# Kernel optimization log

Hardware: AMD Instinct MI355X
Metric: run time of the kernel (lower is better)

Reference implementation:

```python
import jax, jax.numpy as jnp
import numpy as np

NFEAT, NHID, NCLASS = 256, 128, 40
N_NODES, N_EDGES = 50000, 800000
BN_EPS = 1e-5


def setup_inputs() -> dict:
    key = jax.random.key(0)
    ks = jax.random.split(key, 8)
    x = jax.random.normal(ks[0], (N_NODES, NFEAT), dtype=jnp.float32)
    edge_index = jax.random.randint(ks[1], (2, N_EDGES), 0, N_NODES, dtype=jnp.int64)
    # GCNConv layer 0: nfeat -> nhid (Glorot-ish scale)
    W0 = jax.random.normal(ks[2], (NFEAT, NHID), dtype=jnp.float32) / np.sqrt(NFEAT)
    b0 = jnp.zeros((NHID,), dtype=jnp.float32)
    # BatchNorm1d(nhid)
    gamma0 = jnp.ones((NHID,), dtype=jnp.float32)
    beta0 = jnp.zeros((NHID,), dtype=jnp.float32)
    # GCNConv last: nhid -> nclass
    W1 = jax.random.normal(ks[3], (NHID, NCLASS), dtype=jnp.float32) / np.sqrt(NHID)
    b1 = jnp.zeros((NCLASS,), dtype=jnp.float32)
    return {"x": x, "edge_index": edge_index, "W0": W0, "b0": b0,
            "gamma0": gamma0, "beta0": beta0, "W1": W1, "b1": b1}


def _gcn_conv(x, src, dst, W, b, num_nodes):
    # normalize=False GCNConv: linear transform then raw sum aggregation src->dst
    h = x @ W                                   # [N, out]
    out = jax.ops.segment_sum(h[src], dst, num_segments=num_nodes)
    return out + b


def reference(x, edge_index, W0, b0, gamma0, beta0, W1, b1):
    N = x.shape[0]
    src, dst = edge_index[0], edge_index[1]
    # layer 0 conv
    h = _gcn_conv(x, src, dst, W0, b0, N)       # [N, nhid]
    # BatchNorm1d (training-mode batch stats, biased variance)
    mu = h.mean(axis=0)
    var = jnp.mean((h - mu) ** 2, axis=0)
    h = gamma0 * (h - mu) * jax.lax.rsqrt(var + BN_EPS) + beta0
    h = jax.nn.relu(h)
    # (dropout skipped: deterministic eval baseline)
    # last conv (early-return path in original forward)
    out = _gcn_conv(h, src, dst, W1, b1, N)     # [N, nclass]
    return out
```

## Files before the change

kernel.cpp:

```cpp
#include <hip/hip_runtime.h>
#include <hip/hip_fp8.h>

#define NFEAT 256
#define NHID 128
#define NCLASS 40
#define NNODES 50000
#define NEDGES 800000
#define BN_EPS 1e-5f
#define NBK 196
#define NBLK 100
#define EPB 8000
#define NW1 6250
#define GEMM1_BLOCKS 1563

typedef __attribute__((ext_vector_type(4))) float f32x4;
typedef __attribute__((ext_vector_type(8))) short bf16x8;

__device__ inline ushort f2bf(float f) {
    uint u = __float_as_uint(f);
    u += 0x7FFF + ((u >> 16) & 1);
    return (ushort)(u >> 16);
}
__device__ inline float bflo(uint v) { return __uint_as_float(v << 16); }
__device__ inline float bfhi(uint v) { return __uint_as_float(v & 0xFFFF0000u); }

__device__ inline uint pk_fp8x4(float a0, float a1, float a2, float a3) {
#if __has_builtin(__builtin_amdgcn_cvt_pk_fp8_f32)
    int u = 0;
    u = __builtin_amdgcn_cvt_pk_fp8_f32(a0, a1, u, false);
    u = __builtin_amdgcn_cvt_pk_fp8_f32(a2, a3, u, true);
    return (uint)u;
#else
    __hip_fp8_e4m3 q0(a0), q1(a1), q2(a2), q3(a3);
    return (uint)q0.__x | ((uint)q1.__x << 8) | ((uint)q2.__x << 16) | ((uint)q3.__x << 24);
#endif
}
__device__ inline float fp8lo(uint v) {
#if __has_builtin(__builtin_amdgcn_cvt_f32_fp8)
    return __builtin_amdgcn_cvt_f32_fp8((int)v, 0);
#else
    __hip_fp8_e4m3 q; q.__x = (__hip_fp8_storage_t)(v & 0xFF); return (float)q;
#endif
}
__device__ inline float fp8hi(uint v) {
#if __has_builtin(__builtin_amdgcn_cvt_f32_fp8)
    return __builtin_amdgcn_cvt_f32_fp8((int)v, 1);
#else
    __hip_fp8_e4m3 q; q.__x = (__hip_fp8_storage_t)((v >> 8) & 0xFF); return (float)q;
#endif
}

__global__ void k_prep(const float* __restrict__ W0, ushort* __restrict__ W0F,
                       const int* __restrict__ ei, int* __restrict__ bcnt,
                       float* __restrict__ stats, int* __restrict__ rowptr) {
    __shared__ int cnt[NBK];
    if (blockIdx.x < 16) {
        if (blockIdx.x == 0) {
            stats[threadIdx.x] = 0.f;
            if (threadIdx.x == 0) rowptr[NNODES] = NEDGES;
        }
        const int t = blockIdx.x * 256 + threadIdx.x;
        const int lane = t & 63;
        const int grp = t >> 6;
        const int kc = grp & 7, fi = grp >> 3;
        const int n = fi * 16 + (lane & 15);
        const int k0 = kc * 32 + (lane >> 4) * 8;
        ushort v[8];
        #pragma unroll
        for (int j = 0; j < 8; ++j) v[j] = f2bf(W0[(k0 + j) * NHID + n]);
        uint4 u;
        u.x = (uint)v[0] | ((uint)v[1] << 16);
        u.y = (uint)v[2] | ((uint)v[3] << 16);
        u.z = (uint)v[4] | ((uint)v[5] << 16);
        u.w = (uint)v[6] | ((uint)v[7] << 16);
        *(uint4*)&W0F[(grp * 64 + lane) * 8] = u;
    } else {
        const int blk = blockIdx.x - 16;
        const int t = threadIdx.x;
        if (t < NBK) cnt[t] = 0;
        __syncthreads();
        const int base = blk * EPB;
        for (int i = t; i < EPB; i += 256)
            atomicAdd(&cnt[ei[NEDGES + base + i] >> 8], 1);
        __syncthreads();
        if (t < NBK) bcnt[blk * NBK + t] = cnt[t];
    }
}

__launch_bounds__(256, 1)
__global__ void k_scatter_gemm1(const int* __restrict__ ei, const int* __restrict__ bcnt,
                                uint* __restrict__ packed,
                                const float* __restrict__ x, const ushort* __restrict__ W0F,
                                uchar* __restrict__ h1) {
    __shared__ int s_sc[256], s_cur[256];
    if (blockIdx.x < NBLK) {
        const int tid = threadIdx.x, blk = blockIdx.x;
        int tot = 0, pre = 0;
        if (tid < NBK) {
            for (int bb = 0; bb < NBLK; ++bb) {
                const int v = bcnt[bb * NBK + tid];
                tot += v;
                if (bb < blk) pre += v;
            }
        }
        s_sc[tid] = tot;
        __syncthreads();
        for (int o = 1; o < 256; o <<= 1) {
            const int v = (tid >= o) ? s_sc[tid - o] : 0;
            __syncthreads();
            s_sc[tid] += v;
            __syncthreads();
        }
        s_cur[tid] = (s_sc[tid] - tot) + pre;
        __syncthreads();
        const int base = blk * EPB;
        for (int i = tid; i < EPB; i += 256) {
            const int src = ei[base + i];
            const int dst = ei[NEDGES + base + i];
            const int pos = atomicAdd(&s_cur[dst >> 8], 1);
            packed[pos] = (uint)src | ((uint)(dst & 255) << 16);
        }
    } else {
        const int gt = (blockIdx.x - NBLK) * 256 + threadIdx.x;
        const int w = gt >> 6;
        if (w >= NW1) return;
        const int lane = gt & 63;
        const int half = w & 1;
        const int node = (w >> 1) * 16 + (lane & 15);
        const int nclamp = node < NNODES ? node : NNODES - 1;
        const float* xg = &x[(long)nclamp * NFEAT + (lane >> 4) * 8];

        float4 xa[8], xb[8];
        #pragma unroll
        for (int kc = 0; kc < 8; ++kc) {
            xa[kc] = *(const float4*)(xg + kc * 32);
            xb[kc] = *(const float4*)(xg + kc * 32 + 4);
        }
        __builtin_amdgcn_sched_barrier(0);
        bf16x8 xf[8];
        #pragma unroll
        for (int kc = 0; kc < 8; ++kc) {
            xf[kc][0]=(short)f2bf(xa[kc].x); xf[kc][1]=(short)f2bf(xa[kc].y);
            xf[kc][2]=(short)f2bf(xa[kc].z); xf[kc][3]=(short)f2bf(xa[kc].w);
            xf[kc][4]=(short)f2bf(xb[kc].x); xf[kc][5]=(short)f2bf(xb[kc].y);
            xf[kc][6]=(short)f2bf(xb[kc].z); xf[kc][7]=(short)f2bf(xb[kc].w);
        }
        __builtin_amdgcn_sched_barrier(0);
        f32x4 acc[4];
        #pragma unroll
        for (int f = 0; f < 4; ++f) acc[f] = (f32x4){0.f, 0.f, 0.f, 0.f};
        const ushort* wbase = &W0F[(size_t)lane * 8];
        #pragma unroll
        for (int kc = 0; kc < 8; ++kc) {
            #pragma unroll
            for (int f = 0; f < 4; ++f) {
                const int grp = (half * 4 + f) * 8 + kc;
                const bf16x8 wf = *(const bf16x8*)&wbase[(size_t)grp * 64 * 8];
                acc[f] = __builtin_amdgcn_mfma_f32_16x16x32_bf16(wf, xf[kc], acc[f], 0, 0, 0);
            }
        }
        if (node < NNODES) {
            const int nq = (lane >> 4) * 4;
            uchar* hp = &h1[(long)node * NHID + half * 64 + nq];
            #pragma unroll
            for (int f = 0; f < 4; ++f)
                *(uint*)&hp[f * 16] = pk_fp8x4(acc[f][0], acc[f][1], acc[f][2], acc[f][3]);
        }
    }
}

__launch_bounds__(256)
__global__ void k_bksort(const uint* __restrict__ packed, const int* __restrict__ bcnt,
                         int* __restrict__ esrc, int* __restrict__ rowptr) {
    __shared__ int s_cnt[256], s_sc[256], s_cur[256];
    __shared__ int s_seg[2];
    const int b = blockIdx.x, tid = threadIdx.x;
    int tot = 0;
    if (tid < NBK)
        for (int bb = 0; bb < NBLK; ++bb) tot += bcnt[bb * NBK + tid];
    s_sc[tid] = tot;
    __syncthreads();
    for (int o = 1; o < 256; o <<= 1) {
        const int v = (tid >= o) ? s_sc[tid - o] : 0;
        __syncthreads();
        s_sc[tid] += v;
        __syncthreads();
    }
    if (tid == b) { s_seg[0] = s_sc[b] - tot; s_seg[1] = s_sc[b]; }
    __syncthreads();
    const int nb = s_seg[0], ne = s_seg[1], n = ne - nb;
    s_cnt[tid] = 0;
    __syncthreads();
    for (int i = tid; i < n; i += 256)
        atomicAdd(&s_cnt[packed[nb + i] >> 16], 1);
    __syncthreads();
    const int v = s_cnt[tid];
    s_sc[tid] = v;
    __syncthreads();
    for (int o = 1; o < 256; o <<= 1) {
        const int tmp = (tid >= o) ? s_sc[tid - o] : 0;
        __syncthreads();
        s_sc[tid] += tmp;
        __syncthreads();
    }
    const int excl = s_sc[tid] - v;
    s_cur[tid] = excl;
    const int node = (b << 8) + tid;
    if (node < NNODES) rowptr[node] = nb + excl;
    __syncthreads();
    for (int i = tid; i < n; i += 256) {
        const uint p = packed[nb + i];
        const int pos = atomicAdd(&s_cur[p >> 16], 1);
        esrc[nb + pos] = (int)(p & 0xFFFFu);
    }
}

__launch_bounds__(256)
__global__ void k_gather1(const int* __restrict__ rowptr, const int* __restrict__ esrc,
                          const uchar* __restrict__ h1, const float* __restrict__ b0,
                          ushort* __restrict__ agg1bf) {
    const int w = (blockIdx.x * blockDim.x + threadIdx.x) >> 6;
    const int lane = threadIdx.x & 63;
    if (w >= NNODES) return;
    const int beg = rowptr[w], end = rowptr[w + 1];
    const int f = lane * 2;
    float2 acc = *(const float2*)&b0[f];
    int i = beg;
    for (; i + 7 < end; i += 8) {
        uint v[8];
        #pragma unroll
        for (int j = 0; j < 8; ++j)
            v[j] = (uint)*(const ushort*)&h1[(long)esrc[i + j] * NHID + f];
        #pragma unroll
        for (int j = 0; j < 8; ++j) { acc.x += fp8lo(v[j]); acc.y += fp8hi(v[j]); }
    }
    for (; i < end; ++i) {
        const uint v = (uint)*(const ushort*)&h1[(long)esrc[i] * NHID + f];
        acc.x += fp8lo(v); acc.y += fp8hi(v);
    }
    const uint u = (uint)f2bf(acc.x) | ((uint)f2bf(acc.y) << 16);
    *(uint*)&agg1bf[(long)w * NHID + f] = u;
}

__global__ void k_bnstats(const ushort* __restrict__ agg1bf,
                          float* __restrict__ sums, float* __restrict__ sumsq) {
    __shared__ float sd[256 * 8], sd2[256 * 8];
    const int t = threadIdx.x;
    const int c8 = (t & 15) * 8;
    const int rr = t >> 4;
    float s[8] = {}, q[8] = {};
    for (int r = blockIdx.x * 16 + rr; r < NNODES; r += gridDim.x * 16) {
        const uint4 u = *(const uint4*)&agg1bf[(long)r * NHID + c8];
        const uint uu[4] = {u.x, u.y, u.z, u.w};
        #pragma unroll
        for (int j = 0; j < 4; ++j) {
            const float a0 = bflo(uu[j]), a1 = bfhi(uu[j]);
            s[2 * j] += a0; s[2 * j + 1] += a1;
            q[2 * j] += a0 * a0; q[2 * j + 1] += a1 * a1;
        }
    }
    #pragma unroll
    for (int j = 0; j < 8; ++j) { sd[t * 8 + j] = s[j]; sd2[t * 8 + j] = q[j]; }
    __syncthreads();
    if (t < 128) {
        const int g = t >> 3, j = t & 7;
        float ss = 0.f, qq = 0.f;
        #pragma unroll
        for (int r = 0; r < 16; ++r) {
            ss += sd[(r * 16 + g) * 8 + j];
            qq += sd2[(r * 16 + g) * 8 + j];
        }
        atomicAdd(&sums[g * 8 + j], ss);
        atomicAdd(&sumsq[g * 8 + j], qq);
    }
}

__launch_bounds__(256)
__global__ void k_gemm2(const ushort* __restrict__ agg1bf, const float* __restrict__ W1,
                        const float* __restrict__ sums, const float* __restrict__ sumsq,
                        const float* __restrict__ gamma, const float* __restrict__ beta,
                        ushort* __restrict__ h2) {
    __shared__ float xs[64 * 132];
    __shared__ float wt[40 * 132];
    __shared__ float s_scale[128], s_shift[128];
    const int t = threadIdx.x;
    const int base = blockIdx.x * 64;

    if (t < NHID) {
        const float mu = sums[t] * (1.f / NNODES);
        float var = sumsq[t] * (1.f / NNODES) - mu * mu;
        var = fmaxf(var, 0.f);
        const float sc = gamma[t] * rsqrtf(var + BN_EPS);
        s_scale[t] = sc;
        s_shift[t] = beta[t] - mu * sc;
    }
    for (int idx = t; idx < NHID * NCLASS; idx += 256) {
        const int c = idx / NCLASS, j = idx % NCLASS;
        wt[j * 132 + c] = W1[idx];
    }
    __syncthreads();
    {
        const int cc = (t & 15) * 8;
        const int rb = t >> 4;
        #pragma unroll
        for (int p = 0; p < 4; ++p) {
            const int row = p * 16 + rb;
            const int g = base + row;
            uint4 u = make_uint4(0u, 0u, 0u, 0u);
            if (g < NNODES) u = *(const uint4*)&agg1bf[(long)g * NHID + cc];
            const uint uu[4] = {u.x, u.y, u.z, u.w};
            #pragma unroll
            for (int q = 0; q < 4; ++q) {
                const int c0 = cc + q * 2;
                const float a0 = bflo(uu[q]), a1 = bfhi(uu[q]);
                xs[row * 132 + c0]     = fmaxf(a0 * s_scale[c0]     + s_shift[c0],     0.f);
                xs[row * 132 + c0 + 1] = fmaxf(a1 * s_scale[c0 + 1] + s_shift[c0 + 1], 0.f);
            }
        }
    }
    __syncthreads();

    const int node = t >> 2;
    const int j0 = (t & 3) * 10;
    float acc[10] = {};
    for (int c4 = 0; c4 < 32; ++c4) {
        const int c = c4 * 4;
        const float4 a = *(const float4*)&xs[node * 132 + c];
        #pragma unroll
        for (int jj = 0; jj < 10; ++jj) {
            const float4 wv = *(const float4*)&wt[(j0 + jj) * 132 + c];
            acc[jj] += a.x * wv.x + a.y * wv.y + a.z * wv.z + a.w * wv.w;
        }
    }
    const int g = base + node;
    if (g < NNODES) {
        #pragma unroll
        for (int p = 0; p < 5; ++p) {
            uint u = (uint)f2bf(acc[2 * p]) | ((uint)f2bf(acc[2 * p + 1]) << 16);
            *(uint*)&h2[(long)g * NCLASS + j0 + 2 * p] = u;
        }
    }
}

__launch_bounds__(256)
__global__ void k_gather2(const int* __restrict__ rowptr, const int* __restrict__ esrc,
                          const ushort* __restrict__ h2, const float* __restrict__ b1,
                          float* __restrict__ out) {
    const int t = threadIdx.x;
    if (t >= 240) return;
    const int node = blockIdx.x * 12 + t / 20;
    if (node >= NNODES) return;
    const int f = (t % 20) * 2;
    const int beg = rowptr[node], end = rowptr[node + 1];
    float2 acc = make_float2(b1[f], b1[f + 1]);
    int i = beg;
    for (; i + 3 < end; i += 4) {
        const uint v0 = *(const uint*)&h2[(long)esrc[i]     * NCLASS + f];
        const uint v1 = *(const uint*)&h2[(long)esrc[i + 1] * NCLASS + f];
        const uint v2 = *(const uint*)&h2[(long)esrc[i + 2] * NCLASS + f];
        const uint v3 = *(const uint*)&h2[(long)esrc[i + 3] * NCLASS + f];
        acc.x += (bflo(v0) + bflo(v1)) + (bflo(v2) + bflo(v3));
        acc.y += (bfhi(v0) + bfhi(v1)) + (bfhi(v2) + bfhi(v3));
    }
    for (; i < end; ++i) {
        const uint v = *(const uint*)&h2[(long)esrc[i] * NCLASS + f];
        acc.x += bflo(v); acc.y += bfhi(v);
    }
    *(float2*)&out[(long)node * NCLASS + f] = acc;
}

extern "C" void kernel_launch(void* const* d_in, const int* in_sizes, int n_in,
                              void* d_out, int out_size, void* d_ws, size_t ws_size,
                              hipStream_t stream) {
    const float* x      = (const float*)d_in[0];
    const int*   ei     = (const int*)d_in[1];
    const float* W0     = (const float*)d_in[2];
    const float* b0     = (const float*)d_in[3];
    const float* gamma0 = (const float*)d_in[4];
    const float* beta0  = (const float*)d_in[5];
    const float* W1     = (const float*)d_in[6];
    const float* b1     = (const float*)d_in[7];
    float* out = (float*)d_out;

    char* ws = (char*)d_ws;
    float* sums  = (float*)ws;
    float* sumsq = sums + 128;
    int* wsI     = (int*)(ws + 4096);
    int* rowptr  = wsI;
    int* esrc    = wsI + 50048;
    int* bcnt    = wsI + 850048;
    ushort* W0F  = (ushort*)(ws + 3563520);
    uchar* h1    = (uchar*)(ws + 3629056);
    ushort* agg1bf = (ushort*)(ws + 16429056);
    uint* packed = (uint*)agg1bf;
    ushort* h2   = (ushort*)h1;

    k_prep<<<16 + NBLK, 256, 0, stream>>>(W0, W0F, ei, bcnt, sums, rowptr);
    k_scatter_gemm1<<<NBLK + GEMM1_BLOCKS, 256, 0, stream>>>(ei, bcnt, packed, x, W0F, h1);
    k_bksort<<<NBK, 256, 0, stream>>>(packed, bcnt, esrc, rowptr);
    k_gather1<<<(NNODES * 64 + 255) / 256, 256, 0, stream>>>(rowptr, esrc, h1, b0, agg1bf);
    k_bnstats<<<256, 256, 0, stream>>>(agg1bf, sums, sumsq);
    k_gemm2<<<(NNODES + 63) / 64, 256, 0, stream>>>(agg1bf, W1, sums, sumsq, gamma0, beta0, h2);
    k_gather2<<<(NNODES + 11) / 12, 256, 0, stream>>>(rowptr, esrc, h2, b1, out);
}
```

Before: 148.4 us.

## Co-schedule GEMM1 with bucket sort and make GEMM1 persistent with register-resident weights

The edge scatter now runs as its own small kernel, and GEMM1 is fused with the per-bucket sort instead of the scatter. The GEMM1 blocks become persistent waves (512 blocks) that load their half of W0 into registers once and loop over node tiles, which removes repeated weight reloads. The intent is to hide the latency-bound sort behind GEMM1 work and cut weight traffic. The cost is heavy register use (32 bf16x8 fragments per lane), which could lower occupancy, and the scatter now runs alone with only 100 blocks.

```diff
diff --git a/kernel.cpp b/kernel.cpp
--- a/kernel.cpp
+++ b/kernel.cpp
@@ -11,7 +11,8 @@
 #define NBLK 100
 #define EPB 8000
 #define NW1 6250
-#define GEMM1_BLOCKS 1563
+#define G1R_BLOCKS 512
+#define G1R_WAVES (G1R_BLOCKS * 4)
 
 typedef __attribute__((ext_vector_type(4))) float f32x4;
 typedef __attribute__((ext_vector_type(8))) short bf16x8;
@@ -87,22 +88,49 @@
     }
 }
 
-__launch_bounds__(256, 1)
-__global__ void k_scatter_gemm1(const int* __restrict__ ei, const int* __restrict__ bcnt,
-                                uint* __restrict__ packed,
-                                const float* __restrict__ x, const ushort* __restrict__ W0F,
-                                uchar* __restrict__ h1) {
+__global__ void k_scatter(const int* __restrict__ ei, const int* __restrict__ bcnt,
+                          uint* __restrict__ packed) {
     __shared__ int s_sc[256], s_cur[256];
-    if (blockIdx.x < NBLK) {
-        const int tid = threadIdx.x, blk = blockIdx.x;
-        int tot = 0, pre = 0;
-        if (tid < NBK) {
-            for (int bb = 0; bb < NBLK; ++bb) {
-                const int v = bcnt[bb * NBK + tid];
-                tot += v;
-                if (bb < blk) pre += v;
-            }
-        }
+    const int tid = threadIdx.x, blk = blockIdx.x;
+    int tot = 0, pre = 0;
+    if (tid < NBK) {
+        for (int bb = 0; bb < NBLK; ++bb) {
+            const int v = bcnt[bb * NBK + tid];
+            tot += v;
+            if (bb < blk) pre += v;
+        }
+    }
+    s_sc[tid] = tot;
+    __syncthreads();
+    for (int o = 1; o < 256; o <<= 1) {
+        const int v = (tid >= o) ? s_sc[tid - o] : 0;
+        __syncthreads();
+        s_sc[tid] += v;
+        __syncthreads();
+    }
+    s_cur[tid] = (s_sc[tid] - tot) + pre;
+    __syncthreads();
+    const int base = blk * EPB;
+    for (int i = tid; i < EPB; i += 256) {
+        const int src = ei[base + i];
+        const int dst = ei[NEDGES + base + i];
+        const int pos = atomicAdd(&s_cur[dst >> 8], 1);
+        packed[pos] = (uint)src | ((uint)(dst & 255) << 16);
+    }
+}
+
+__launch_bounds__(256)
+__global__ void k_sort_gemm1(const uint* __restrict__ packed, const int* __restrict__ bcnt,
+                             int* __restrict__ esrc, int* __restrict__ rowptr,
+                             const float* __restrict__ x, const ushort* __restrict__ W0F,
+                             uchar* __restrict__ h1) {
+    __shared__ int s_cnt[256], s_sc[256], s_cur[256];
+    __shared__ int s_seg[2];
+    if (blockIdx.x < NBK) {
+        const int b = blockIdx.x, tid = threadIdx.x;
+        int tot = 0;
+        if (tid < NBK)
+            for (int bb = 0; bb < NBLK; ++bb) tot += bcnt[bb * NBK + tid];
         s_sc[tid] = tot;
         __syncthreads();
         for (int o = 1; o < 256; o <<= 1) {
@@ -111,107 +139,85 @@
             s_sc[tid] += v;
             __syncthreads();
         }
-        s_cur[tid] = (s_sc[tid] - tot) + pre;
-        __syncthreads();
-        const int base = blk * EPB;
-        for (int i = tid; i < EPB; i += 256) {
-            const int src = ei[base + i];
-            const int dst = ei[NEDGES + base + i];
-            const int pos = atomicAdd(&s_cur[dst >> 8], 1);
-            packed[pos] = (uint)src | ((uint)(dst & 255) << 16);
+        if (tid == b) { s_seg[0] = s_sc[b] - tot; s_seg[1] = s_sc[b]; }
+        __syncthreads();
+        const int nb = s_seg[0], ne = s_seg[1], n = ne - nb;
+        s_cnt[tid] = 0;
+        __syncthreads();
+        for (int i = tid; i < n; i += 256)
+            atomicAdd(&s_cnt[packed[nb + i] >> 16], 1);
+        __syncthreads();
+        const int v = s_cnt[tid];
+        s_sc[tid] = v;
+        __syncthreads();
+        for (int o = 1; o < 256; o <<= 1) {
+            const int tmp = (tid >= o) ? s_sc[tid - o] : 0;
+            __syncthreads();
+            s_sc[tid] += tmp;
+            __syncthreads();
+        }
+        const int excl = s_sc[tid] - v;
+        s_cur[tid] = excl;
+        const int node = (b << 8) + tid;
+        if (node < NNODES) rowptr[node] = nb + excl;
+        __syncthreads();
+        for (int i = tid; i < n; i += 256) {
+            const uint p = packed[nb + i];
+            const int pos = atomicAdd(&s_cur[p >> 16], 1);
+            esrc[nb + pos] = (int)(p & 0xFFFFu);
         }
     } else {
-        const int gt = (blockIdx.x - NBLK) * 256 + threadIdx.x;
-        const int w = gt >> 6;
-        if (w >= NW1) return;
-        const int lane = gt & 63;
-        const int half = w & 1;
-        const int node = (w >> 1) * 16 + (lane & 15);
-        const int nclamp = node < NNODES ? node : NNODES - 1;
-        const float* xg = &x[(long)nclamp * NFEAT + (lane >> 4) * 8];
-
-        float4 xa[8], xb[8];
-        #pragma unroll
-        for (int kc = 0; kc < 8; ++kc) {
-            xa[kc] = *(const float4*)(xg + kc * 32);
-            xb[kc] = *(const float4*)(xg + kc * 32 + 4);
-        }
-        __builtin_amdgcn_sched_barrier(0);
-        bf16x8 xf[8];
-        #pragma unroll
-        for (int kc = 0; kc < 8; ++kc) {
-            xf[kc][0]=(short)f2bf(xa[kc].x); xf[kc][1]=(short)f2bf(xa[kc].y);
-            xf[kc][2]=(short)f2bf(xa[kc].z); xf[kc][3]=(short)f2bf(xa[kc].w);
-            xf[kc][4]=(short)f2bf(xb[kc].x); xf[kc][5]=(short)f2bf(xb[kc].y);
-            xf[kc][6]=(short)f2bf(xb[kc].z); xf[kc][7]=(short)f2bf(xb[kc].w);
-        }
-        __builtin_amdgcn_sched_barrier(0);
-        f32x4 acc[4];
-        #pragma unroll
-        for (int f = 0; f < 4; ++f) acc[f] = (f32x4){0.f, 0.f, 0.f, 0.f};
+        const int wv = threadIdx.x >> 6;
+        const int lane = threadIdx.x & 63;
+        const int W = (blockIdx.x - NBK) * 4 + wv;
+        const int half = W & 1;
         const ushort* wbase = &W0F[(size_t)lane * 8];
-        #pragma unroll
-        for (int kc = 0; kc < 8; ++kc) {
-            #pragma unroll
-            for (int f = 0; f < 4; ++f) {
-                const int grp = (half * 4 + f) * 8 + kc;
-                const bf16x8 wf = *(const bf16x8*)&wbase[(size_t)grp * 64 * 8];
-                acc[f] = __builtin_amdgcn_mfma_f32_16x16x32_bf16(wf, xf[kc], acc[f], 0, 0, 0);
+
+        bf16x8 wf[32];
+        #pragma unroll
+        for (int fi = 0; fi < 4; ++fi)
+            #pragma unroll
+            for (int kc = 0; kc < 8; ++kc)
+                wf[fi * 8 + kc] =
+                    *(const bf16x8*)&wbase[(size_t)(((half * 4 + fi) * 8 + kc) * 64) * 8];
+
+        for (int task = W; task < NW1; task += G1R_WAVES) {
+            const int g = task >> 1;
+            const int node = g * 16 + (lane & 15);
+            const int nclamp = node < NNODES ? node : NNODES - 1;
+            const float* xg = &x[(long)nclamp * NFEAT + (lane >> 4) * 8];
+
+            float4 xa[8], xb[8];
+            #pragma unroll
+            for (int kc = 0; kc < 8; ++kc) {
+                xa[kc] = *(const float4*)(xg + kc * 32);
+                xb[kc] = *(const float4*)(xg + kc * 32 + 4);
             }
-        }
-        if (node < NNODES) {
-            const int nq = (lane >> 4) * 4;
-            uchar* hp = &h1[(long)node * NHID + half * 64 + nq];
-            #pragma unroll
-            for (int f = 0; f < 4; ++f)
-                *(uint*)&hp[f * 16] = pk_fp8x4(acc[f][0], acc[f][1], acc[f][2], acc[f][3]);
-        }
-    }
-}
-
-__launch_bounds__(256)
-__global__ void k_bksort(const uint* __restrict__ packed, const int* __restrict__ bcnt,
-                         int* __restrict__ esrc, int* __restrict__ rowptr) {
-    __shared__ int s_cnt[256], s_sc[256], s_cur[256];
-    __shared__ int s_seg[2];
-    const int b = blockIdx.x, tid = threadIdx.x;
-    int tot = 0;
-    if (tid < NBK)
-        for (int bb = 0; bb < NBLK; ++bb) tot += bcnt[bb * NBK + tid];
-    s_sc[tid] = tot;
-    __syncthreads();
-    for (int o = 1; o < 256; o <<= 1) {
-        const int v = (tid >= o) ? s_sc[tid - o] : 0;
-        __syncthreads();
-        s_sc[tid] += v;
-        __syncthreads();
-    }
-    if (tid == b) { s_seg[0] = s_sc[b] - tot; s_seg[1] = s_sc[b]; }
-    __syncthreads();
-    const int nb = s_seg[0], ne = s_seg[1], n = ne - nb;
-    s_cnt[tid] = 0;
-    __syncthreads();
-    for (int i = tid; i < n; i += 256)
-        atomicAdd(&s_cnt[packed[nb + i] >> 16], 1);
-    __syncthreads();
-    const int v = s_cnt[tid];
-    s_sc[tid] = v;
-    __syncthreads();
-    for (int o = 1; o < 256; o <<= 1) {
-        const int tmp = (tid >= o) ? s_sc[tid - o] : 0;
-        __syncthreads();
-        s_sc[tid] += tmp;
-        __syncthreads();
-    }
-    const int excl = s_sc[tid] - v;
-    s_cur[tid] = excl;
-    const int node = (b << 8) + tid;
-    if (node < NNODES) rowptr[node] = nb + excl;
-    __syncthreads();
-    for (int i = tid; i < n; i += 256) {
-        const uint p = packed[nb + i];
-        const int pos = atomicAdd(&s_cur[p >> 16], 1);
-        esrc[nb + pos] = (int)(p & 0xFFFFu);
+            bf16x8 xf[8];
+            #pragma unroll
+            for (int kc = 0; kc < 8; ++kc) {
+                xf[kc][0]=(short)f2bf(xa[kc].x); xf[kc][1]=(short)f2bf(xa[kc].y);
+                xf[kc][2]=(short)f2bf(xa[kc].z); xf[kc][3]=(short)f2bf(xa[kc].w);
+                xf[kc][4]=(short)f2bf(xb[kc].x); xf[kc][5]=(short)f2bf(xb[kc].y);
+                xf[kc][6]=(short)f2bf(xb[kc].z); xf[kc][7]=(short)f2bf(xb[kc].w);
+            }
+            f32x4 acc[4];
+            #pragma unroll
+            for (int f = 0; f < 4; ++f) acc[f] = (f32x4){0.f, 0.f, 0.f, 0.f};
+            #pragma unroll
+            for (int kc = 0; kc < 8; ++kc)
+                #pragma unroll
+                for (int f = 0; f < 4; ++f)
+                    acc[f] = __builtin_amdgcn_mfma_f32_16x16x32_bf16(wf[f * 8 + kc], xf[kc],
+                                                                     acc[f], 0, 0, 0);
+            if (node < NNODES) {
+                const int nq = (lane >> 4) * 4;
+                uchar* hp = &h1[(long)node * NHID + half * 64 + nq];
+                #pragma unroll
+                for (int f = 0; f < 4; ++f)
+                    *(uint*)&hp[f * 16] = pk_fp8x4(acc[f][0], acc[f][1], acc[f][2], acc[f][3]);
+            }
+        }
     }
 }
 
@@ -396,8 +402,8 @@
     ushort* h2   = (ushort*)h1;
 
     k_prep<<<16 + NBLK, 256, 0, stream>>>(W0, W0F, ei, bcnt, sums, rowptr);
-    k_scatter_gemm1<<<NBLK + GEMM1_BLOCKS, 256, 0, stream>>>(ei, bcnt, packed, x, W0F, h1);
-    k_bksort<<<NBK, 256, 0, stream>>>(packed, bcnt, esrc, rowptr);
+    k_scatter<<<NBLK, 256, 0, stream>>>(ei, bcnt, packed);
+    k_sort_gemm1<<<NBK + G1R_BLOCKS, 256, 0, stream>>>(packed, bcnt, esrc, rowptr, x, W0F, h1);
     k_gather1<<<(NNODES * 64 + 255) / 256, 256, 0, stream>>>(rowptr, esrc, h1, b0, agg1bf);
     k_bnstats<<<256, 256, 0, stream>>>(agg1bf, sums, sumsq);
     k_gemm2<<<(NNODES + 63) / 64, 256, 0, stream>>>(agg1bf, W1, sums, sumsq, gamma0, beta0, h2);
```

New measurement: 142.7 us, median of 2. 1.04x faster.
